# Kernel optimization log

Hardware: AMD Instinct MI355X
Metric: run time of the kernel (lower is better)

Reference implementation:

```python
import jax, jax.numpy as jnp
import numpy as np

D_MODEL = 1024
D_STATE = 128
BATCH = 16
SEQ = 2048
LN_EPS = 1e-5


def setup_inputs() -> dict:
    key = jax.random.key(0)
    ks = jax.random.split(key, 4)
    x = jax.random.normal(ks[0], (BATCH, SEQ, D_MODEL), dtype=jnp.float32)
    A = jax.random.normal(ks[1], (D_STATE, D_STATE), dtype=jnp.float32) * 0.01
    B = jax.random.normal(ks[2], (D_STATE, D_MODEL), dtype=jnp.float32) * 0.01
    C = jax.random.normal(ks[3], (D_MODEL, D_STATE), dtype=jnp.float32) * 0.01
    D = jnp.ones((D_MODEL,), dtype=jnp.float32)
    gamma = jnp.ones((D_MODEL,), dtype=jnp.float32)
    beta = jnp.zeros((D_MODEL,), dtype=jnp.float32)
    return {"x": x, "A": A, "B": B, "C": C, "D": D, "gamma": gamma, "beta": beta}


def reference(x, A, B, C, D, gamma, beta):
    # x: [B, S, d_model]
    bsz, seq, dm = x.shape

    # Precompute input projections for all timesteps in one big matmul:
    # x_t @ B.T for all t -> [B, S, d_state]
    xB = jnp.einsum('bsd,nd->bsn', x, B)

    def step(state, xb_t):
        # state: [B, d_state]; xb_t: [B, d_state]
        state = jnp.tanh(state @ A.T + xb_t)
        return state, state

    init = jnp.zeros((bsz, A.shape[0]), dtype=x.dtype)
    # scan over time: xB transposed to [S, B, d_state]
    _, states = jax.lax.scan(step, init, jnp.swapaxes(xB, 0, 1))
    states = jnp.swapaxes(states, 0, 1)  # [B, S, d_state]

    # out_t = state_t @ C.T + D * x_t (batched over all t)
    out = jnp.einsum('bsn,dn->bsd', states, C) + D * x

    # LayerNorm(out + x); dropout is identity in eval mode
    y = out + x
    mu = jnp.mean(y, axis=-1, keepdims=True)
    var = jnp.mean(jnp.square(y - mu), axis=-1, keepdims=True)
    return (y - mu) * jax.lax.rsqrt(var + LN_EPS) * gamma + beta
```

## Files before the change

### kernel.cpp

```cpp
#include <hip/hip_runtime.h>
#include <stdint.h>


#define D_MODEL 1024
#define D_STATE 128
#define BATCH   16
#define SEQ     2048
#define NTOK    (BATCH*SEQ)

#define WIN   4
#define LOOK  12
#define NSTEP (WIN+LOOK)

typedef __bf16 bf16x8 __attribute__((ext_vector_type(8)));
typedef float  f32x4  __attribute__((ext_vector_type(4)));

__device__ __forceinline__ f32x4 mfma16(bf16x8 a, bf16x8 b, f32x4 c){
  return __builtin_amdgcn_mfma_f32_16x16x32_bf16(a, b, c, 0, 0, 0);
}

__device__ __forceinline__ bf16x8 to_bf8(float4 a, float4 b){
  bf16x8 r;
  r[0]=(__bf16)a.x; r[1]=(__bf16)a.y; r[2]=(__bf16)a.z; r[3]=(__bf16)a.w;
  r[4]=(__bf16)b.x; r[5]=(__bf16)b.y; r[6]=(__bf16)b.z; r[7]=(__bf16)b.w;
  return r;
}

__device__ __forceinline__ uint32_t pk2(float a, float b){
  uint32_t lo = (uint32_t)__builtin_bit_cast(unsigned short, (__bf16)a);
  uint32_t hi = (uint32_t)__builtin_bit_cast(unsigned short, (__bf16)b);
  return lo | (hi << 16);
}

__device__ __forceinline__ float tanh_fast(float x){
  float e = __expf(2.f*x);
  return fmaf(-2.f, __builtin_amdgcn_rcpf(e + 1.f), 1.f);
}

#define GLDS16(g,l) __builtin_amdgcn_global_load_lds( \
    (const __attribute__((address_space(1))) void*)(g), \
    (__attribute__((address_space(3))) void*)(l), 16, 0, 0)

__global__ __launch_bounds__(512, 2)
void k1_xb(const float* __restrict__ x, const float* __restrict__ Bm,
           float* __restrict__ xb){
  __shared__ __align__(16) float lx[2][16*1024];
  const int tid = threadIdx.x;
  const int w = tid >> 6;
  const int l = tid & 63;
  const int q = l >> 4, c = l & 15;

  bf16x8 Bf[32];
  {
    const float* rowp = Bm + (size_t)(w*16 + c)*D_MODEL;
    #pragma unroll
    for(int kc=0; kc<32; kc++){
      const float* p = rowp + kc*32 + q*8;
      Bf[kc] = to_bf8(*(const float4*)p, *(const float4*)(p+4));
    }
  }

  const int tile0 = blockIdx.x * 8;

  {
    const char* src = (const char*)(x + (size_t)tile0*16*D_MODEL);
    #pragma unroll
    for(int i=0; i<8; i++){
      const int r = w*2 + (i>>2);
      const int j = (i&3)*64 + l;
      GLDS16(src + (size_t)r*4096 + 16*(j ^ (r&7)),
             &lx[0][(w*8192 + i*1024)>>2]);
    }
  }
  __syncthreads();

  for(int j8=0; j8<8; j8++){
    const int buf = j8 & 1;
    if(j8+1 < 8){
      const char* src = (const char*)(x + (size_t)(tile0+j8+1)*16*D_MODEL);
      #pragma unroll
      for(int i=0; i<8; i++){
        const int r = w*2 + (i>>2);
        const int jb = (i&3)*64 + l;
        GLDS16(src + (size_t)r*4096 + 16*(jb ^ (r&7)),
               &lx[buf^1][(w*8192 + i*1024)>>2]);
      }
    }
    f32x4 a0 = (f32x4){0.f,0.f,0.f,0.f};
    f32x4 a1 = (f32x4){0.f,0.f,0.f,0.f};
    const int h = c & 7;
    const float* base = &lx[buf][c*1024];
    #pragma unroll
    for(int kc=0; kc<32; kc+=2){
      const int g0 = kc*8 + 2*q;
      float4 x0 = *(const float4*)&base[4*((g0  ) ^ h)];
      float4 x1 = *(const float4*)&base[4*((g0+1) ^ h)];
      a0 = mfma16(to_bf8(x0, x1), Bf[kc], a0);
      const int g1 = (kc+1)*8 + 2*q;
      float4 x2 = *(const float4*)&base[4*((g1  ) ^ h)];
      float4 x3 = *(const float4*)&base[4*((g1+1) ^ h)];
      a1 = mfma16(to_bf8(x2, x3), Bf[kc+1], a1);
    }
    #pragma unroll
    for(int r=0; r<4; r++){
      const int tok = (tile0+j8)*16 + q*4 + r;
      xb[(size_t)tok*D_STATE + w*16 + c] = a0[r] + a1[r];
    }
    __syncthreads();
  }
}

__global__ __launch_bounds__(64, 1)
void k2_scan(const float* __restrict__ xb, const float* __restrict__ Am,
             uint32_t* __restrict__ st){
  __shared__ __align__(16) uint16_t lA[128*136];
  __shared__ __align__(16) uint32_t Tl[16*68];
  const int l = threadIdx.x;
  const int q = l >> 4;
  const int b = l & 15;
  const int w = blockIdx.x;
  const int t0 = w*WIN - LOOK;

  for(int i0 = l*4; i0 < D_STATE*D_STATE; i0 += 256){
    const int r = i0 >> 7, k = i0 & 127;
    float4 v = *(const float4*)&Am[i0];
    *(uint2*)&lA[r*136 + k] = make_uint2(pk2(v.x,v.y), pk2(v.z,v.w));
  }
  __syncthreads();

  bf16x8 Bf[4];
  #pragma unroll
  for(int kc=0; kc<4; kc++){
    #pragma unroll
    for(int e=0; e<8; e++) Bf[kc][e] = (__bf16)0.f;
  }

  float4 cur[8], nxt[8];
  {
    const int t = t0;
    if(t >= 0 && t < SEQ){
      const float* p = xb + ((size_t)b*SEQ + t)*D_STATE;
      #pragma unroll
      for(int t8=0; t8<8; t8++) cur[t8] = *(const float4*)(p + t8*16 + q*4);
    } else {
      #pragma unroll
      for(int t8=0; t8<8; t8++) cur[t8] = (float4){0.f,0.f,0.f,0.f};
    }
  }

  for(int i=0; i<NSTEP; i++){
    const int t = t0 + i;
    const int t1 = t + 1;
    if(t1 >= 0 && t1 < SEQ){
      const float* p = xb + ((size_t)b*SEQ + t1)*D_STATE;
      #pragma unroll
      for(int t8=0; t8<8; t8++) nxt[t8] = *(const float4*)(p + t8*16 + q*4);
    } else {
      #pragma unroll
      for(int t8=0; t8<8; t8++) nxt[t8] = (float4){0.f,0.f,0.f,0.f};
    }
    const bool real = (t >= w*WIN);
    #pragma unroll
    for(int t8=0; t8<8; t8++){
      const uint16_t* ap = &lA[(t8*16 + b)*136];
      f32x4 d = (f32x4){cur[t8].x, cur[t8].y, cur[t8].z, cur[t8].w};
      #pragma unroll
      for(int kc=0; kc<4; kc++){
        bf16x8 af = __builtin_bit_cast(bf16x8, *(const uint4*)&ap[kc*32 + q*8]);
        d = mfma16(af, Bf[kc], d);
      }
      float s0 = tanh_fast(d[0]);
      float s1 = tanh_fast(d[1]);
      float s2 = tanh_fast(d[2]);
      float s3 = tanh_fast(d[3]);
      uint32_t p01 = pk2(s0, s1), p23 = pk2(s2, s3);
      *(uint2*)&Tl[b*68 + t8*8 + q*2] = make_uint2(p01, p23);
      if(real){
        *(uint2*)&st[((size_t)b*SEQ + t)*64 + t8*8 + q*2] = make_uint2(p01, p23);
      }
    }
    asm volatile("s_waitcnt lgkmcnt(0)" ::: "memory");
    #pragma unroll
    for(int kc=0; kc<4; kc++){
      uint4 u = *(const uint4*)&Tl[b*68 + kc*16 + q*4];
      Bf[kc] = __builtin_bit_cast(bf16x8, u);
    }
    #pragma unroll
    for(int t8=0; t8<8; t8++) cur[t8] = nxt[t8];
  }
}

__global__ __launch_bounds__(512, 2)
void k3_out(const uint32_t* __restrict__ st, const float* __restrict__ Cm,
            const float* __restrict__ x, const float* __restrict__ Dv,
            const float* __restrict__ gv, const float* __restrict__ bv,
            float* __restrict__ out){
  __shared__ __align__(16) float pl[3][1024];
  __shared__ __align__(16) float p1s[2][16*8], p2s[2][16*8];
  const int tid = threadIdx.x;
  const int w = tid >> 6;
  const int l = tid & 63;
  const int q = l >> 4, c = l & 15;

  bf16x8 Cf[8][4];
  #pragma unroll
  for(int nt=0; nt<8; nt++){
    const float* rowp = Cm + (size_t)(w*128 + nt*16 + c)*D_STATE;
    #pragma unroll
    for(int kc=0; kc<4; kc++){
      const float* p = rowp + kc*32 + q*8;
      Cf[nt][kc] = to_bf8(*(const float4*)p, *(const float4*)(p+4));
    }
  }

  for(int i = tid; i < 768; i += 512){
    const int a = i >> 8, o = (i & 255)*4;
    const float* src = (a==0) ? Dv : (a==1) ? gv : bv;
    float4 v = *(const float4*)&src[o];
    if(a == 0){ v.x += 1.f; v.y += 1.f; v.z += 1.f; v.w += 1.f; }
    *(float4*)&pl[a][o] = v;
  }
  __syncthreads();

  #pragma unroll
  for(int j=0; j<8; j++){
    const int m0 = blockIdx.x*128 + j*16;

    bf16x8 Sf[4];
    #pragma unroll
    for(int kc=0; kc<4; kc++){
      uint4 u = *(const uint4*)&st[(size_t)(m0 + c)*64 + kc*16 + q*4];
      Sf[kc] = __builtin_bit_cast(bf16x8, u);
    }
    float4 xr[8];
    #pragma unroll
    for(int nt=0; nt<8; nt++){
      xr[nt] = *(const float4*)&x[(size_t)(m0 + c)*D_MODEL + w*128 + nt*16 + q*4];
    }

    f32x4 acc[8];
    #pragma unroll
    for(int nt=0; nt<8; nt++){
      f32x4 d4 = (f32x4){0.f,0.f,0.f,0.f};
      #pragma unroll
      for(int kc=0; kc<4; kc++) d4 = mfma16(Cf[nt][kc], Sf[kc], d4);
      acc[nt] = d4;
    }

    float s1 = 0.f, s2 = 0.f;
    #pragma unroll
    for(int nt=0; nt<8; nt++){
      const float4 dd4 = *(const float4*)&pl[0][w*128 + nt*16 + q*4];
      const float4 xv = xr[nt];
      float y0 = fmaf(dd4.x, xv.x, acc[nt][0]);
      float y1 = fmaf(dd4.y, xv.y, acc[nt][1]);
      float y2 = fmaf(dd4.z, xv.z, acc[nt][2]);
      float y3 = fmaf(dd4.w, xv.w, acc[nt][3]);
      acc[nt][0] = y0; acc[nt][1] = y1; acc[nt][2] = y2; acc[nt][3] = y3;
      s1 += (y0 + y1) + (y2 + y3);
      s2 = fmaf(y0, y0, s2); s2 = fmaf(y1, y1, s2);
      s2 = fmaf(y2, y2, s2); s2 = fmaf(y3, y3, s2);
    }
    s1 += __shfl_xor(s1, 16); s2 += __shfl_xor(s2, 16);
    s1 += __shfl_xor(s1, 32); s2 += __shfl_xor(s2, 32);
    if(l < 16){
      p1s[j&1][l*8 + w] = s1;
      p2s[j&1][l*8 + w] = s2;
    }
    asm volatile("s_waitcnt lgkmcnt(0)" ::: "memory");
    __builtin_amdgcn_s_barrier();

    float4 u0 = *(const float4*)&p1s[j&1][c*8];
    float4 u1 = *(const float4*)&p1s[j&1][c*8 + 4];
    float4 v0 = *(const float4*)&p2s[j&1][c*8];
    float4 v1 = *(const float4*)&p2s[j&1][c*8 + 4];
    const float a  = ((u0.x+u0.y)+(u0.z+u0.w)) + ((u1.x+u1.y)+(u1.z+u1.w));
    const float b2 = ((v0.x+v0.y)+(v0.z+v0.w)) + ((v1.x+v1.y)+(v1.z+v1.w));
    const float mu  = a * (1.f/1024.f);
    const float var = b2 * (1.f/1024.f) - mu*mu;
    const float rs  = __builtin_amdgcn_rsqf(var + 1e-5f);

    float* orow = out + (size_t)(m0 + c)*D_MODEL + w*128;
    #pragma unroll
    for(int nt=0; nt<8; nt++){
      const float4 gg4 = *(const float4*)&pl[1][w*128 + nt*16 + q*4];
      const float4 bb4 = *(const float4*)&pl[2][w*128 + nt*16 + q*4];
      float4 o4;
      o4.x = (acc[nt][0] - mu)*rs*gg4.x + bb4.x;
      o4.y = (acc[nt][1] - mu)*rs*gg4.y + bb4.y;
      o4.z = (acc[nt][2] - mu)*rs*gg4.z + bb4.z;
      o4.w = (acc[nt][3] - mu)*rs*gg4.w + bb4.w;
      *(float4*)&orow[nt*16 + q*4] = o4;
    }
  }
}

extern "C" void kernel_launch(void* const* d_in, const int* in_sizes, int n_in,
                              void* d_out, int out_size, void* d_ws, size_t ws_size,
                              hipStream_t stream){
  const float* x  = (const float*)d_in[0];
  const float* Am = (const float*)d_in[1];
  const float* Bm = (const float*)d_in[2];
  const float* Cm = (const float*)d_in[3];
  const float* Dv = (const float*)d_in[4];
  const float* gv = (const float*)d_in[5];
  const float* bv = (const float*)d_in[6];
  float* out = (float*)d_out;

  float*    xb = (float*)d_ws;
  uint32_t* st = (uint32_t*)((char*)d_ws + (size_t)NTOK*D_STATE*4);

  k1_xb <<<NTOK/128, 512, 0, stream>>>(x, Bm, xb);
  k2_scan<<<SEQ/WIN,  64, 0, stream>>>(xb, Am, st);
  k3_out <<<NTOK/128, 512, 0, stream>>>(st, Cm, x, Dv, gv, bv, out);
}
```

Measured before the change: 365.6 us.

## Double-buffer x and state tiles into LDS in output kernel, relax k1 barriers

The output/LayerNorm kernel now prefetches the next 16-token tile of x and the bf16 states into swizzled, double-buffered LDS using global_load_lds. Explicit vmcnt waits and raw barriers replace the per-thread direct global loads, so HBM reads overlap the MFMA and LayerNorm work. The xB projection kernel also swaps __syncthreads for targeted vmcnt/lgkmcnt waits plus s_barrier, letting its prefetch stay in flight across the barrier. The risk is that the roughly 140 KB of added LDS in the output kernel may limit it to one block per CU, and the hand-counted vmcnt values are fragile.

```diff
diff --git a/kernel.cpp b/kernel.cpp
--- a/kernel.cpp
+++ b/kernel.cpp
@@ -40,6 +40,9 @@
 #define GLDS16(g,l) __builtin_amdgcn_global_load_lds( \
     (const __attribute__((address_space(1))) void*)(g), \
     (__attribute__((address_space(3))) void*)(l), 16, 0, 0)
+#define GLDS4(g,l) __builtin_amdgcn_global_load_lds( \
+    (const __attribute__((address_space(1))) void*)(g), \
+    (__attribute__((address_space(3))) void*)(l), 4, 0, 0)
 
 __global__ __launch_bounds__(512, 2)
 void k1_xb(const float* __restrict__ x, const float* __restrict__ Bm,
@@ -72,11 +75,11 @@
              &lx[0][(w*8192 + i*1024)>>2]);
     }
   }
-  __syncthreads();
+  asm volatile("" ::: "memory");
 
   for(int j8=0; j8<8; j8++){
     const int buf = j8 & 1;
-    if(j8+1 < 8){
+    if(j8 < 7){
       const char* src = (const char*)(x + (size_t)(tile0+j8+1)*16*D_MODEL);
       #pragma unroll
       for(int i=0; i<8; i++){
@@ -85,7 +88,12 @@
         GLDS16(src + (size_t)r*4096 + 16*(jb ^ (r&7)),
                &lx[buf^1][(w*8192 + i*1024)>>2]);
       }
-    }
+      asm volatile("s_waitcnt vmcnt(8)" ::: "memory");
+    } else {
+      asm volatile("s_waitcnt vmcnt(0)" ::: "memory");
+    }
+    __builtin_amdgcn_s_barrier();
+
     f32x4 a0 = (f32x4){0.f,0.f,0.f,0.f};
     f32x4 a1 = (f32x4){0.f,0.f,0.f,0.f};
     const int h = c & 7;
@@ -106,7 +114,9 @@
       const int tok = (tile0+j8)*16 + q*4 + r;
       xb[(size_t)tok*D_STATE + w*16 + c] = a0[r] + a1[r];
     }
-    __syncthreads();
+    asm volatile("s_waitcnt lgkmcnt(0)" ::: "memory");
+    __builtin_amdgcn_s_barrier();
+    asm volatile("" ::: "memory");
   }
 }
 
@@ -195,12 +205,15 @@
             const float* __restrict__ x, const float* __restrict__ Dv,
             const float* __restrict__ gv, const float* __restrict__ bv,
             float* __restrict__ out){
+  __shared__ __align__(16) float    lx[2][16*1024];
+  __shared__ __align__(16) uint32_t lst[2][16*64];
   __shared__ __align__(16) float pl[3][1024];
   __shared__ __align__(16) float p1s[2][16*8], p2s[2][16*8];
   const int tid = threadIdx.x;
   const int w = tid >> 6;
   const int l = tid & 63;
   const int q = l >> 4, c = l & 15;
+  const int h = c & 7;
 
   bf16x8 Cf[8][4];
   #pragma unroll
@@ -222,20 +235,63 @@
   }
   __syncthreads();
 
+  const int tok0 = blockIdx.x*128;
+
+  {
+    const char* xsrc = (const char*)(x + (size_t)tok0*D_MODEL);
+    #pragma unroll
+    for(int i=0; i<8; i++){
+      const int r = w*2 + (i>>2);
+      const int jb = (i&3)*64 + l;
+      GLDS16(xsrc + (size_t)r*4096 + 16*(jb ^ (r&7)),
+             &lx[0][(w*8192 + i*1024)>>2]);
+    }
+    const uint32_t* ssrc = st + (size_t)tok0*64;
+    #pragma unroll
+    for(int e=0; e<2; e++){
+      const int r = w*2 + e;
+      const int src = r*64 + ((((l>>2) ^ (r&7))<<2) | (l&3));
+      GLDS4(ssrc + src, &lst[0][w*128 + e*64]);
+    }
+  }
+  asm volatile("" ::: "memory");
+
   #pragma unroll
   for(int j=0; j<8; j++){
-    const int m0 = blockIdx.x*128 + j*16;
+    const int buf = j & 1;
+    const int m0 = tok0 + j*16;
+
+    if(j < 7){
+      const int m1 = m0 + 16;
+      const char* xsrc = (const char*)(x + (size_t)m1*D_MODEL);
+      #pragma unroll
+      for(int i=0; i<8; i++){
+        const int r = w*2 + (i>>2);
+        const int jb = (i&3)*64 + l;
+        GLDS16(xsrc + (size_t)r*4096 + 16*(jb ^ (r&7)),
+               &lx[buf^1][(w*8192 + i*1024)>>2]);
+      }
+      const uint32_t* ssrc = st + (size_t)m1*64;
+      #pragma unroll
+      for(int e=0; e<2; e++){
+        const int r = w*2 + e;
+        const int src = r*64 + ((((l>>2) ^ (r&7))<<2) | (l&3));
+        GLDS4(ssrc + src, &lst[buf^1][w*128 + e*64]);
+      }
+    }
+    asm volatile("" ::: "memory");
+
+    if(j == 0)      asm volatile("s_waitcnt vmcnt(10)" ::: "memory");
+    else if(j < 7)  asm volatile("s_waitcnt vmcnt(18)" ::: "memory");
+    else            asm volatile("s_waitcnt vmcnt(8)"  ::: "memory");
+    __builtin_amdgcn_s_barrier();
 
     bf16x8 Sf[4];
+    const char* sb = (const char*)&lst[buf][0] + c*256;
     #pragma unroll
     for(int kc=0; kc<4; kc++){
-      uint4 u = *(const uint4*)&st[(size_t)(m0 + c)*64 + kc*16 + q*4];
+      uint4 u = *(const uint4*)(sb + 16*(((kc<<2)|q) ^ h));
       Sf[kc] = __builtin_bit_cast(bf16x8, u);
-    }
-    float4 xr[8];
-    #pragma unroll
-    for(int nt=0; nt<8; nt++){
-      xr[nt] = *(const float4*)&x[(size_t)(m0 + c)*D_MODEL + w*128 + nt*16 + q*4];
     }
 
     f32x4 acc[8];
@@ -247,11 +303,12 @@
       acc[nt] = d4;
     }
 
+    const char* xbse = (const char*)&lx[buf][0] + c*4096;
     float s1 = 0.f, s2 = 0.f;
     #pragma unroll
     for(int nt=0; nt<8; nt++){
+      const float4 xv  = *(const float4*)(xbse + 16*((w*32 + nt*4 + q) ^ h));
       const float4 dd4 = *(const float4*)&pl[0][w*128 + nt*16 + q*4];
-      const float4 xv = xr[nt];
       float y0 = fmaf(dd4.x, xv.x, acc[nt][0]);
       float y1 = fmaf(dd4.y, xv.y, acc[nt][1]);
       float y2 = fmaf(dd4.z, xv.z, acc[nt][2]);
@@ -264,16 +321,16 @@
     s1 += __shfl_xor(s1, 16); s2 += __shfl_xor(s2, 16);
     s1 += __shfl_xor(s1, 32); s2 += __shfl_xor(s2, 32);
     if(l < 16){
-      p1s[j&1][l*8 + w] = s1;
-      p2s[j&1][l*8 + w] = s2;
+      p1s[buf][l*8 + w] = s1;
+      p2s[buf][l*8 + w] = s2;
     }
     asm volatile("s_waitcnt lgkmcnt(0)" ::: "memory");
     __builtin_amdgcn_s_barrier();
 
-    float4 u0 = *(const float4*)&p1s[j&1][c*8];
-    float4 u1 = *(const float4*)&p1s[j&1][c*8 + 4];
-    float4 v0 = *(const float4*)&p2s[j&1][c*8];
-    float4 v1 = *(const float4*)&p2s[j&1][c*8 + 4];
+    float4 u0 = *(const float4*)&p1s[buf][c*8];
+    float4 u1 = *(const float4*)&p1s[buf][c*8 + 4];
+    float4 v0 = *(const float4*)&p2s[buf][c*8];
+    float4 v1 = *(const float4*)&p2s[buf][c*8 + 4];
     const float a  = ((u0.x+u0.y)+(u0.z+u0.w)) + ((u1.x+u1.y)+(u1.z+u1.w));
     const float b2 = ((v0.x+v0.y)+(v0.z+v0.w)) + ((v1.x+v1.y)+(v1.z+v1.w));
     const float mu  = a * (1.f/1024.f);
@@ -292,6 +349,7 @@
       o4.w = (acc[nt][3] - mu)*rs*gg4.w + bb4.w;
       *(float4*)&orow[nt*16 + q*4] = o4;
     }
+    asm volatile("" ::: "memory");
   }
 }
 
```

New measurement: 355.4 us. 1.03x faster.
